# Optimization experiments

Hardware: AMD Instinct MI355X
Metric: run time of the kernel (lower is better)

## Reference

```python
import jax, jax.numpy as jnp
import numpy as np

D_MODEL = 2048
N_EXPERTS = 64
TOP_K = 2


def setup_inputs() -> dict:
    key = jax.random.key(0)
    kx, kw, kb = jax.random.split(key, 3)
    x = jax.random.normal(kx, (4, 8192, D_MODEL), dtype=jnp.float32)
    # nn.Linear(input_size, n_experts): weight [n_experts, input_size], bias [n_experts]
    W = jax.random.normal(kw, (N_EXPERTS, D_MODEL), dtype=jnp.float32) * (1.0 / np.sqrt(D_MODEL))
    b = jax.random.normal(kb, (N_EXPERTS,), dtype=jnp.float32) * 0.01
    return {"x": x, "W": W, "b": b}


def reference(x, W, b):
    B, S, D = x.shape
    # logits over experts: [B, S, E]
    logits = jnp.einsum("bsd,ed->bse", x, W) + b
    probs = jax.nn.softmax(logits, axis=-1)
    # top-k along experts (sorted descending, matching torch.topk)
    top_w, top_idx = jax.lax.top_k(probs, TOP_K)
    return top_idx, top_w
```

## Files before the change

### kernel.cpp

```cpp
#include <hip/hip_runtime.h>
#include <stdint.h>

#define D_MODEL 2048
#define N_EXP   64
#define TOKS    32
#define WAVES   4
#define KW      (D_MODEL / WAVES)
#define KS      64
#define NS      (KW / KS)
#define ROW_F4  16

__global__ void make_Wq2(const float* __restrict__ W, float* __restrict__ Wq2) {
    int o  = blockIdx.x * 256 + threadIdx.x;
    int i  = o & 3;
    int eg = (o >> 2) & 7;
    int j  = (o >> 5) & 7;
    int kq = o >> 8;
    Wq2[o] = W[(8 * j + eg) * D_MODEL + 4 * kq + i];
}

union SMemU {
    float4 xs[WAVES * TOKS * ROW_F4];
    float  red[2][TOKS * 65];
};

__global__ __launch_bounds__(256, 4)
void router_d(const float* __restrict__ x, const float4* __restrict__ Wq2,
              const float* __restrict__ bias, float* __restrict__ out, int n_tokens)
{
    __shared__ SMemU sm;
    const int tid  = threadIdx.x;
    const int lane = tid & 63;
    const int wv   = tid >> 6;
    const int tg   = lane >> 3;
    const int eg   = lane & 7;
    const int tok0 = blockIdx.x * TOKS;
    const int kw   = wv * KW;

    const int trow = lane >> 4;
    const int c    = lane & 15;

    float acc[4][8];
    #pragma unroll
    for (int tt = 0; tt < 4; ++tt)
        #pragma unroll
        for (int j = 0; j < 8; ++j) acc[tt][j] = 0.f;

    float4* ldsbase = sm.xs + wv * (TOKS * ROW_F4);

    for (int s = 0; s < NS; ++s) {
        const int kb = kw + s * KS;
        #pragma unroll
        for (int it = 0; it < 8; ++it) {
            const int t  = 4 * it + trow;
            const int gc = c ^ (t & 7);
            const float* gp = x + (size_t)(tok0 + t) * D_MODEL + kb + 4 * gc;
            float4* lp = ldsbase + it * 64;
            __builtin_amdgcn_global_load_lds(
                (const __attribute__((address_space(1))) void*)gp,
                (__attribute__((address_space(3))) void*)lp, 16, 0, 0);
        }
        asm volatile("s_waitcnt vmcnt(0)" ::: "memory");
        #pragma unroll
        for (int q = 0; q < KS / 4; ++q) {
            const int kq = (kb >> 2) + q;
            float4 xv[4];
            #pragma unroll
            for (int tt = 0; tt < 4; ++tt) {
                const int t = 8 * tt + tg;
                xv[tt] = ldsbase[(size_t)t * ROW_F4 + (q ^ tg)];
            }
            const float4* wp = Wq2 + (size_t)kq * 64 + eg;
            #pragma unroll
            for (int j = 0; j < 8; ++j) {
                const float4 w4 = wp[8 * j];
                #pragma unroll
                for (int tt = 0; tt < 4; ++tt) {
                    acc[tt][j] = fmaf(w4.x, xv[tt].x, acc[tt][j]);
                    acc[tt][j] = fmaf(w4.y, xv[tt].y, acc[tt][j]);
                    acc[tt][j] = fmaf(w4.z, xv[tt].z, acc[tt][j]);
                    acc[tt][j] = fmaf(w4.w, xv[tt].w, acc[tt][j]);
                }
            }
        }
    }

    __syncthreads();
    if (wv >= 2) {
        float* R = sm.red[wv - 2];
        #pragma unroll
        for (int tt = 0; tt < 4; ++tt)
            #pragma unroll
            for (int j = 0; j < 8; ++j)
                R[(8 * tt + tg) * 65 + 8 * j + eg] = acc[tt][j];
    }
    __syncthreads();
    if (wv < 2) {
        const float* R = sm.red[wv];
        #pragma unroll
        for (int tt = 0; tt < 4; ++tt)
            #pragma unroll
            for (int j = 0; j < 8; ++j)
                acc[tt][j] += R[(8 * tt + tg) * 65 + 8 * j + eg];
    }
    __syncthreads();
    if (wv == 1) {
        float* R = sm.red[0];
        #pragma unroll
        for (int tt = 0; tt < 4; ++tt)
            #pragma unroll
            for (int j = 0; j < 8; ++j)
                R[(8 * tt + tg) * 65 + 8 * j + eg] = acc[tt][j];
    }
    __syncthreads();

    if (wv == 0) {
        const float* R = sm.red[0];
        float bj[8];
        #pragma unroll
        for (int j = 0; j < 8; ++j) bj[j] = bias[8 * j + eg];
        float* ow = out + 2 * (size_t)n_tokens;

        #pragma unroll
        for (int tt = 0; tt < 4; ++tt) {
            float v[8];
            #pragma unroll
            for (int j = 0; j < 8; ++j)
                v[j] = acc[tt][j] + R[(8 * tt + tg) * 65 + 8 * j + eg] + bj[j];
            float v1 = v[0]; int i1 = eg;
            float v2 = -3.4e38f; int i2 = 1 << 20;
            #pragma unroll
            for (int j = 1; j < 8; ++j) {
                const int e = 8 * j + eg;
                if (v[j] > v1)      { v2 = v1; i2 = i1; v1 = v[j]; i1 = e; }
                else if (v[j] > v2) { v2 = v[j]; i2 = e; }
            }
            #pragma unroll
            for (int m = 1; m < 8; m <<= 1) {
                float b1 = __shfl_xor(v1, m, 64); int j1 = __shfl_xor(i1, m, 64);
                float b2 = __shfl_xor(v2, m, 64); int j2 = __shfl_xor(i2, m, 64);
                bool aw = (v1 > b1) || (v1 == b1 && i1 < j1);
                float lw_v = aw ? b1 : v1;  int lw_i = aw ? j1 : i1;
                float ws_v = aw ? v2 : b2;  int ws_i = aw ? i2 : j2;
                float nv1  = aw ? v1 : b1;  int ni1  = aw ? i1 : j1;
                bool sw = (lw_v > ws_v) || (lw_v == ws_v && lw_i < ws_i);
                v1 = nv1;               i1 = ni1;
                v2 = sw ? lw_v : ws_v;  i2 = sw ? lw_i : ws_i;
            }
            float ssum = 0.f;
            #pragma unroll
            for (int j = 0; j < 8; ++j) ssum += __expf(v[j] - v1);
            #pragma unroll
            for (int m = 1; m < 8; m <<= 1) ssum += __shfl_xor(ssum, m, 64);
            const float inv = 1.0f / ssum;
            const float w1  = inv;
            const float w2  = __expf(v2 - v1) * inv;

            if (eg == tt) {
                const int g = tok0 + 8 * tt + tg;
                float2 fi; fi.x = (float)i1; fi.y = (float)i2;
                ((float2*)out)[g] = fi;
                float2 fw; fw.x = w1; fw.y = w2;
                ((float2*)ow)[g] = fw;
            }
        }
    }
}

extern "C" void kernel_launch(void* const* d_in, const int* in_sizes, int n_in,
                              void* d_out, int out_size, void* d_ws, size_t ws_size,
                              hipStream_t stream) {
    const float* x = (const float*)d_in[0];
    const float* W = (const float*)d_in[1];
    const float* b = (const float*)d_in[2];
    float* out = (float*)d_out;
    float* Wq2 = (float*)d_ws;
    const int n_tokens = in_sizes[0] / D_MODEL;

    make_Wq2<<<(D_MODEL * N_EXP) / 256, 256, 0, stream>>>(W, Wq2);
    router_d<<<n_tokens / TOKS, 256, 0, stream>>>(x, (const float4*)Wq2, b, out, n_tokens);
}
```

Before: 487.5 us.

## Double-buffer x staging in LDS to overlap global loads with FMA compute

Splits each wave's k-range into smaller 32-wide stages held in two LDS buffers per wave, with a matching swizzle. The next stage's async global_load_lds is issued before computing on the current one, and a partial vmcnt wait lets the prefetch stay in flight. This targets the full-drain stall that previously followed every stage, at the cost of more loop iterations and reliance on vmcnt counting being correct alongside the W loads.

```diff
diff --git a/kernel.cpp b/kernel.cpp
--- a/kernel.cpp
+++ b/kernel.cpp
@@ -6,9 +6,10 @@
 #define TOKS    32
 #define WAVES   4
 #define KW      (D_MODEL / WAVES)
-#define KS      64
-#define NS      (KW / KS)
-#define ROW_F4  16
+#define KSS     32
+#define NSS     (KW / KSS)
+#define ROW_F4  8
+#define BUF_F4  (TOKS * ROW_F4)
 
 __global__ void make_Wq2(const float* __restrict__ W, float* __restrict__ Wq2) {
     int o  = blockIdx.x * 256 + threadIdx.x;
@@ -20,7 +21,7 @@
 }
 
 union SMemU {
-    float4 xs[WAVES * TOKS * ROW_F4];
+    float4 xs[2 * WAVES * BUF_F4];
     float  red[2][TOKS * 65];
 };
 
@@ -37,8 +38,9 @@
     const int tok0 = blockIdx.x * TOKS;
     const int kw   = wv * KW;
 
-    const int trow = lane >> 4;
-    const int c    = lane & 15;
+    const int trow = lane >> 3;
+    const int c    = lane & 7;
+    const int gc   = c ^ trow;
 
     float acc[4][8];
     #pragma unroll
@@ -46,29 +48,40 @@
         #pragma unroll
         for (int j = 0; j < 8; ++j) acc[tt][j] = 0.f;
 
-    float4* ldsbase = sm.xs + wv * (TOKS * ROW_F4);
+    float4* b0 = sm.xs + (0 * WAVES + wv) * BUF_F4;
+    float4* b1 = sm.xs + (1 * WAVES + wv) * BUF_F4;
 
-    for (int s = 0; s < NS; ++s) {
-        const int kb = kw + s * KS;
+    auto stage = [&](int s, float4* lb) {
+        const int kb = kw + s * KSS;
         #pragma unroll
-        for (int it = 0; it < 8; ++it) {
-            const int t  = 4 * it + trow;
-            const int gc = c ^ (t & 7);
+        for (int it = 0; it < 4; ++it) {
+            const int t = 8 * it + trow;
             const float* gp = x + (size_t)(tok0 + t) * D_MODEL + kb + 4 * gc;
-            float4* lp = ldsbase + it * 64;
             __builtin_amdgcn_global_load_lds(
                 (const __attribute__((address_space(1))) void*)gp,
-                (__attribute__((address_space(3))) void*)lp, 16, 0, 0);
+                (__attribute__((address_space(3))) void*)(lb + it * 64), 16, 0, 0);
         }
-        asm volatile("s_waitcnt vmcnt(0)" ::: "memory");
+    };
+
+    stage(0, b0);
+
+    for (int s = 0; s < NSS; ++s) {
+        float4* cb = (s & 1) ? b1 : b0;
+        if (s + 1 < NSS) {
+            stage(s + 1, (s & 1) ? b0 : b1);
+            asm volatile("s_waitcnt vmcnt(4)" ::: "memory");
+        } else {
+            asm volatile("s_waitcnt vmcnt(0)" ::: "memory");
+        }
+        const int kb = kw + s * KSS;
         #pragma unroll
-        for (int q = 0; q < KS / 4; ++q) {
+        for (int q = 0; q < KSS / 4; ++q) {
             const int kq = (kb >> 2) + q;
             float4 xv[4];
             #pragma unroll
             for (int tt = 0; tt < 4; ++tt) {
                 const int t = 8 * tt + tg;
-                xv[tt] = ldsbase[(size_t)t * ROW_F4 + (q ^ tg)];
+                xv[tt] = cb[(size_t)t * ROW_F4 + (q ^ tg)];
             }
             const float4* wp = Wq2 + (size_t)kq * 64 + eg;
             #pragma unroll
```

New measurement: 467.0 us. 4.2% less time.

## Double-buffer x and W tiles in LDS with 64-token blocks

Applied to the files above, without the earlier changes.

Restructures the router GEMM so each block handles 64 tokens and walks the full K dimension in 32 chunks. The x and a swizzled copy of W are both staged into LDS with asynchronous global-to-LDS loads and double buffering, so the next chunk's loads overlap the current chunk's FMAs. Waves now split K within a chunk instead of owning a fixed K quarter. The goal is to hide global-load latency and halve W re-reads per token. The cost is more accumulator registers, 64 KB of LDS per block, and fewer resident blocks per CU.

```diff
diff --git a/kernel.cpp b/kernel.cpp
--- a/kernel.cpp
+++ b/kernel.cpp
@@ -3,29 +3,28 @@
 
 #define D_MODEL 2048
 #define N_EXP   64
-#define TOKS    32
-#define WAVES   4
-#define KW      (D_MODEL / WAVES)
-#define KS      64
-#define NS      (KW / KS)
-#define ROW_F4  16
-
-__global__ void make_Wq2(const float* __restrict__ W, float* __restrict__ Wq2) {
-    int o  = blockIdx.x * 256 + threadIdx.x;
-    int i  = o & 3;
-    int eg = (o >> 2) & 7;
-    int j  = (o >> 5) & 7;
-    int kq = o >> 8;
-    Wq2[o] = W[(8 * j + eg) * D_MODEL + 4 * kq + i];
+#define TOKS    64
+#define NCHUNK  32
+#define CQ      16
+#define QW      4
+
+__global__ void make_Wq3(const float* __restrict__ W, float* __restrict__ Wq3) {
+    int o   = blockIdx.x * 256 + threadIdx.x;
+    int i   = o & 3;
+    int col = (o >> 2) & 15;
+    int e   = (o >> 6) & 63;
+    int c   = o >> 12;
+    int qL  = (col & 8) | ((col & 7) ^ (e & 7));
+    Wq3[o]  = W[e * D_MODEL + 4 * (c * 16 + qL) + i];
 }
 
 union SMemU {
-    float4 xs[WAVES * TOKS * ROW_F4];
-    float  red[2][TOKS * 65];
+    struct { float4 xs[2][TOKS * CQ]; float4 ws[2][N_EXP * CQ]; } st;
+    float red[2][TOKS * 65];
 };
 
-__global__ __launch_bounds__(256, 4)
-void router_d(const float* __restrict__ x, const float4* __restrict__ Wq2,
+__global__ __launch_bounds__(256, 2)
+void router_d(const float* __restrict__ x, const float4* __restrict__ Wq3,
               const float* __restrict__ bias, float* __restrict__ out, int n_tokens)
 {
     __shared__ SMemU sm;
@@ -35,47 +34,68 @@
     const int tg   = lane >> 3;
     const int eg   = lane & 7;
     const int tok0 = blockIdx.x * TOKS;
-    const int kw   = wv * KW;
-
-    const int trow = lane >> 4;
-    const int c    = lane & 15;
-
-    float acc[4][8];
+
+    const int sl_t4 = lane >> 4;
+    const int sl_c  = lane & 15;
+
+    float acc[8][8];
     #pragma unroll
-    for (int tt = 0; tt < 4; ++tt)
+    for (int tt = 0; tt < 8; ++tt)
         #pragma unroll
         for (int j = 0; j < 8; ++j) acc[tt][j] = 0.f;
 
-    float4* ldsbase = sm.xs + wv * (TOKS * ROW_F4);
-
-    for (int s = 0; s < NS; ++s) {
-        const int kb = kw + s * KS;
-        #pragma unroll
-        for (int it = 0; it < 8; ++it) {
-            const int t  = 4 * it + trow;
-            const int gc = c ^ (t & 7);
-            const float* gp = x + (size_t)(tok0 + t) * D_MODEL + kb + 4 * gc;
-            float4* lp = ldsbase + it * 64;
+    auto stage_x = [&](int c, float4* xb) {
+        #pragma unroll
+        for (int it = 0; it < 4; ++it) {
+            const int i2 = wv * 4 + it;
+            const int t  = i2 * 4 + sl_t4;
+            const int qL = (sl_c & 8) | ((sl_c & 7) ^ (t & 7));
+            const float* gp = x + (size_t)(tok0 + t) * D_MODEL + c * 64 + 4 * qL;
+            float4* lp = xb + i2 * 64;
             __builtin_amdgcn_global_load_lds(
                 (const __attribute__((address_space(1))) void*)gp,
                 (__attribute__((address_space(3))) void*)lp, 16, 0, 0);
         }
+    };
+    auto stage_w = [&](int c, float4* wb) {
+        #pragma unroll
+        for (int iw = 0; iw < 4; ++iw) {
+            const int i2 = wv * 4 + iw;
+            const float4* gp = Wq3 + (size_t)c * 1024 + i2 * 64 + lane;
+            float4* lp = wb + i2 * 64;
+            __builtin_amdgcn_global_load_lds(
+                (const __attribute__((address_space(1))) void*)gp,
+                (__attribute__((address_space(3))) void*)lp, 16, 0, 0);
+        }
+    };
+
+    stage_x(0, sm.st.xs[0]);
+    stage_w(0, sm.st.ws[0]);
+
+    for (int c = 0; c < NCHUNK; ++c) {
         asm volatile("s_waitcnt vmcnt(0)" ::: "memory");
-        #pragma unroll
-        for (int q = 0; q < KS / 4; ++q) {
-            const int kq = (kb >> 2) + q;
-            float4 xv[4];
-            #pragma unroll
-            for (int tt = 0; tt < 4; ++tt) {
-                const int t = 8 * tt + tg;
-                xv[tt] = ldsbase[(size_t)t * ROW_F4 + (q ^ tg)];
-            }
-            const float4* wp = Wq2 + (size_t)kq * 64 + eg;
+        __syncthreads();
+        if (c + 1 < NCHUNK) {
+            stage_x(c + 1, sm.st.xs[(c + 1) & 1]);
+            stage_w(c + 1, sm.st.ws[(c + 1) & 1]);
+        }
+        const float4* xb = sm.st.xs[c & 1];
+        const float4* wb = sm.st.ws[c & 1];
+        #pragma unroll
+        for (int q = 0; q < QW; ++q) {
+            const int qh   = wv * QW + q;
+            const int xcol = (qh & 8) | ((qh & 7) ^ tg);
+            float4 xv[8];
+            #pragma unroll
+            for (int tt = 0; tt < 8; ++tt)
+                xv[tt] = xb[(8 * tt + tg) * CQ + xcol];
             #pragma unroll
             for (int j = 0; j < 8; ++j) {
-                const float4 w4 = wp[8 * j];
+                const int e    = 8 * j + eg;
+                const int wcol = (qh & 8) | ((qh & 7) ^ eg);
+                const float4 w4 = wb[e * CQ + wcol];
                 #pragma unroll
-                for (int tt = 0; tt < 4; ++tt) {
+                for (int tt = 0; tt < 8; ++tt) {
                     acc[tt][j] = fmaf(w4.x, xv[tt].x, acc[tt][j]);
                     acc[tt][j] = fmaf(w4.y, xv[tt].y, acc[tt][j]);
                     acc[tt][j] = fmaf(w4.z, xv[tt].z, acc[tt][j]);
@@ -89,7 +109,7 @@
     if (wv >= 2) {
         float* R = sm.red[wv - 2];
         #pragma unroll
-        for (int tt = 0; tt < 4; ++tt)
+        for (int tt = 0; tt < 8; ++tt)
             #pragma unroll
             for (int j = 0; j < 8; ++j)
                 R[(8 * tt + tg) * 65 + 8 * j + eg] = acc[tt][j];
@@ -98,7 +118,7 @@
     if (wv < 2) {
         const float* R = sm.red[wv];
         #pragma unroll
-        for (int tt = 0; tt < 4; ++tt)
+        for (int tt = 0; tt < 8; ++tt)
             #pragma unroll
             for (int j = 0; j < 8; ++j)
                 acc[tt][j] += R[(8 * tt + tg) * 65 + 8 * j + eg];
@@ -107,7 +127,7 @@
     if (wv == 1) {
         float* R = sm.red[0];
         #pragma unroll
-        for (int tt = 0; tt < 4; ++tt)
+        for (int tt = 0; tt < 8; ++tt)
             #pragma unroll
             for (int j = 0; j < 8; ++j)
                 R[(8 * tt + tg) * 65 + 8 * j + eg] = acc[tt][j];
@@ -122,7 +142,7 @@
         float* ow = out + 2 * (size_t)n_tokens;
 
         #pragma unroll
-        for (int tt = 0; tt < 4; ++tt) {
+        for (int tt = 0; tt < 8; ++tt) {
             float v[8];
             #pragma unroll
             for (int j = 0; j < 8; ++j)
@@ -174,9 +194,9 @@
     const float* W = (const float*)d_in[1];
     const float* b = (const float*)d_in[2];
     float* out = (float*)d_out;
-    float* Wq2 = (float*)d_ws;
+    float* Wq3 = (float*)d_ws;
     const int n_tokens = in_sizes[0] / D_MODEL;
 
-    make_Wq2<<<(D_MODEL * N_EXP) / 256, 256, 0, stream>>>(W, Wq2);
-    router_d<<<n_tokens / TOKS, 256, 0, stream>>>(x, (const float4*)Wq2, b, out, n_tokens);
+    make_Wq3<<<(D_MODEL * N_EXP) / 256, 256, 0, stream>>>(W, Wq3);
+    router_d<<<n_tokens / TOKS, 256, 0, stream>>>(x, (const float4*)Wq3, b, out, n_tokens);
 }
```

New measurement: 479.4 us. About the same (-1.7%).

## Double-buffer x and W tiles in LDS and double tokens per block

Applied to the files above, without the earlier changes.

Each block now handles 64 tokens instead of 32, so every weight value it reads feeds twice as many tokens. Both x and the weight tile are now loaded asynchronously into per-wave LDS buffers with global_load_lds. The loads run double-buffered, with a partial vmcnt wait so the next 16-wide k-slice arrives while the current one is computed. The weight layout is simplified to a plain [kq][expert][4] order. In exchange the accumulator tile doubles, which raises register pressure, and launch bounds drop from 4 to 2 blocks per CU, which lowers occupancy.

```diff
diff --git a/kernel.cpp b/kernel.cpp
--- a/kernel.cpp
+++ b/kernel.cpp
@@ -3,29 +3,28 @@
 
 #define D_MODEL 2048
 #define N_EXP   64
-#define TOKS    32
+#define TOKS    64
 #define WAVES   4
 #define KW      (D_MODEL / WAVES)
-#define KS      64
-#define NS      (KW / KS)
-#define ROW_F4  16
+#define SUBK    16
+#define NSUB    (KW / SUBK)
+#define SUBQ    4
 
-__global__ void make_Wq2(const float* __restrict__ W, float* __restrict__ Wq2) {
+__global__ void make_Wq(const float* __restrict__ W, float* __restrict__ Wq) {
     int o  = blockIdx.x * 256 + threadIdx.x;
     int i  = o & 3;
-    int eg = (o >> 2) & 7;
-    int j  = (o >> 5) & 7;
+    int e  = (o >> 2) & 63;
     int kq = o >> 8;
-    Wq2[o] = W[(8 * j + eg) * D_MODEL + 4 * kq + i];
+    Wq[o] = W[e * D_MODEL + 4 * kq + i];
 }
 
 union SMemU {
-    float4 xs[WAVES * TOKS * ROW_F4];
+    float4 st[WAVES][2][2][64 * SUBQ];
     float  red[2][TOKS * 65];
 };
 
-__global__ __launch_bounds__(256, 4)
-void router_d(const float* __restrict__ x, const float4* __restrict__ Wq2,
+__global__ __launch_bounds__(256, 2)
+void router_d(const float* __restrict__ x, const float4* __restrict__ Wq,
               const float* __restrict__ bias, float* __restrict__ out, int n_tokens)
 {
     __shared__ SMemU sm;
@@ -36,46 +35,62 @@
     const int eg   = lane & 7;
     const int tok0 = blockIdx.x * TOKS;
     const int kw   = wv * KW;
+    const int kq0  = wv * (KW / 4);
 
-    const int trow = lane >> 4;
-    const int c    = lane & 15;
+    const int sct = lane >> 2;
+    const int scc = lane & 3;
+    const int sgc = scc ^ (sct & 3);
+    const float*  xrow = x + (size_t)(tok0 + sct) * D_MODEL + 4 * sgc;
+    const float4* wrow = Wq + lane;
 
-    float acc[4][8];
+    float acc[8][8];
     #pragma unroll
-    for (int tt = 0; tt < 4; ++tt)
+    for (int tt = 0; tt < 8; ++tt)
         #pragma unroll
         for (int j = 0; j < 8; ++j) acc[tt][j] = 0.f;
 
-    float4* ldsbase = sm.xs + wv * (TOKS * ROW_F4);
-
-    for (int s = 0; s < NS; ++s) {
-        const int kb = kw + s * KS;
+    auto stage = [&](int c, int buf) {
+        const int kb = kw + c * SUBK;
+        float4* xb = sm.st[wv][buf][0];
+        float4* wb = sm.st[wv][buf][1];
         #pragma unroll
-        for (int it = 0; it < 8; ++it) {
-            const int t  = 4 * it + trow;
-            const int gc = c ^ (t & 7);
-            const float* gp = x + (size_t)(tok0 + t) * D_MODEL + kb + 4 * gc;
-            float4* lp = ldsbase + it * 64;
+        for (int i2 = 0; i2 < 4; ++i2) {
+            const float* gp = xrow + (size_t)(i2 * 16) * D_MODEL + kb;
             __builtin_amdgcn_global_load_lds(
                 (const __attribute__((address_space(1))) void*)gp,
-                (__attribute__((address_space(3))) void*)lp, 16, 0, 0);
+                (__attribute__((address_space(3))) void*)(xb + i2 * 64), 16, 0, 0);
         }
-        asm volatile("s_waitcnt vmcnt(0)" ::: "memory");
         #pragma unroll
-        for (int q = 0; q < KS / 4; ++q) {
-            const int kq = (kb >> 2) + q;
-            float4 xv[4];
+        for (int i2 = 0; i2 < 4; ++i2) {
+            const float4* gp = wrow + (size_t)(kq0 + c * 4 + i2) * 64;
+            __builtin_amdgcn_global_load_lds(
+                (const __attribute__((address_space(1))) void*)gp,
+                (__attribute__((address_space(3))) void*)(wb + i2 * 64), 16, 0, 0);
+        }
+    };
+
+    stage(0, 0);
+
+    for (int c = 0; c < NSUB; ++c) {
+        if (c + 1 < NSUB) {
+            stage(c + 1, (c + 1) & 1);
+            asm volatile("s_waitcnt vmcnt(8)" ::: "memory");
+        } else {
+            asm volatile("s_waitcnt vmcnt(0)" ::: "memory");
+        }
+        const float4* xb = sm.st[wv][c & 1][0];
+        const float4* wb = sm.st[wv][c & 1][1];
+        #pragma unroll
+        for (int q = 0; q < SUBQ; ++q) {
+            float4 xv[8];
             #pragma unroll
-            for (int tt = 0; tt < 4; ++tt) {
-                const int t = 8 * tt + tg;
-                xv[tt] = ldsbase[(size_t)t * ROW_F4 + (q ^ tg)];
-            }
-            const float4* wp = Wq2 + (size_t)kq * 64 + eg;
+            for (int tt = 0; tt < 8; ++tt)
+                xv[tt] = xb[(8 * tt + tg) * 4 + (q ^ (tg & 3))];
             #pragma unroll
             for (int j = 0; j < 8; ++j) {
-                const float4 w4 = wp[8 * j];
+                const float4 w4 = wb[q * 64 + 8 * j + eg];
                 #pragma unroll
-                for (int tt = 0; tt < 4; ++tt) {
+                for (int tt = 0; tt < 8; ++tt) {
                     acc[tt][j] = fmaf(w4.x, xv[tt].x, acc[tt][j]);
                     acc[tt][j] = fmaf(w4.y, xv[tt].y, acc[tt][j]);
                     acc[tt][j] = fmaf(w4.z, xv[tt].z, acc[tt][j]);
@@ -89,7 +104,7 @@
     if (wv >= 2) {
         float* R = sm.red[wv - 2];
         #pragma unroll
-        for (int tt = 0; tt < 4; ++tt)
+        for (int tt = 0; tt < 8; ++tt)
             #pragma unroll
             for (int j = 0; j < 8; ++j)
                 R[(8 * tt + tg) * 65 + 8 * j + eg] = acc[tt][j];
@@ -98,7 +113,7 @@
     if (wv < 2) {
         const float* R = sm.red[wv];
         #pragma unroll
-        for (int tt = 0; tt < 4; ++tt)
+        for (int tt = 0; tt < 8; ++tt)
             #pragma unroll
             for (int j = 0; j < 8; ++j)
                 acc[tt][j] += R[(8 * tt + tg) * 65 + 8 * j + eg];
@@ -107,7 +122,7 @@
     if (wv == 1) {
         float* R = sm.red[0];
         #pragma unroll
-        for (int tt = 0; tt < 4; ++tt)
+        for (int tt = 0; tt < 8; ++tt)
             #pragma unroll
             for (int j = 0; j < 8; ++j)
                 R[(8 * tt + tg) * 65 + 8 * j + eg] = acc[tt][j];
@@ -122,7 +137,7 @@
         float* ow = out + 2 * (size_t)n_tokens;
 
         #pragma unroll
-        for (int tt = 0; tt < 4; ++tt) {
+        for (int tt = 0; tt < 8; ++tt) {
             float v[8];
             #pragma unroll
             for (int j = 0; j < 8; ++j)
@@ -174,9 +189,9 @@
     const float* W = (const float*)d_in[1];
     const float* b = (const float*)d_in[2];
     float* out = (float*)d_out;
-    float* Wq2 = (float*)d_ws;
+    float* Wq = (float*)d_ws;
     const int n_tokens = in_sizes[0] / D_MODEL;
 
-    make_Wq2<<<(D_MODEL * N_EXP) / 256, 256, 0, stream>>>(W, Wq2);
-    router_d<<<n_tokens / TOKS, 256, 0, stream>>>(x, (const float4*)Wq2, b, out, n_tokens);
+    make_Wq<<<(D_MODEL * N_EXP) / 256, 256, 0, stream>>>(W, Wq);
+    router_d<<<n_tokens / TOKS, 256, 0, stream>>>(x, (const float4*)Wq, b, out, n_tokens);
 }
```

Result: faster. 412.0 us (-15.5%).
